# Performance work log

Hardware: AMD Instinct MI355X
Metric: run time of the kernel (lower is better)

## Reference

```python
import jax, jax.numpy as jnp
import numpy as np

N = 50000       # num nodes
E = 400000      # num edges (before self loops)
IN, HID, H, OUT = 128, 64, 4, 64
SLOPE = 0.2     # PyG GATv2Conv default negative_slope


def setup_inputs() -> dict:
    key = jax.random.key(0)
    ks = jax.random.split(key, 14)
    def lin(k, fan_in, fan_out):
        return jax.random.normal(k, (fan_in, fan_out), jnp.float32) / np.sqrt(fan_in)
    return {
        "x": jax.random.normal(ks[0], (N, IN), jnp.float32),
        "edge_index": jax.random.randint(ks[1], (2, E), 0, N, jnp.int32),
        # layer 1: in=IN -> HID per head, H heads, concat
        "Wl1": lin(ks[2], IN, H * HID), "bl1": jnp.zeros((H * HID,), jnp.float32),
        "Wr1": lin(ks[3], IN, H * HID), "br1": jnp.zeros((H * HID,), jnp.float32),
        "att1": jax.random.normal(ks[4], (H, HID), jnp.float32) / np.sqrt(HID),
        "bias1": jnp.zeros((H * HID,), jnp.float32),
        # layer 2: in=H*HID -> OUT, 1 head, concat=False
        "Wl2": lin(ks[5], H * HID, OUT), "bl2": jnp.zeros((OUT,), jnp.float32),
        "Wr2": lin(ks[6], H * HID, OUT), "br2": jnp.zeros((OUT,), jnp.float32),
        "att2": jax.random.normal(ks[7], (1, OUT), jnp.float32) / np.sqrt(OUT),
        "bias2": jnp.zeros((OUT,), jnp.float32),
    }


def gatv2_conv(x, src, dst, Wl, bl, Wr, br, att, heads, out_ch, num_nodes):
    """PyG GATv2Conv (share_weights=False). src->dst aggregation at dst."""
    xl = (x @ Wl + bl).reshape(-1, heads, out_ch)  # source transform (x_j)
    xr = (x @ Wr + br).reshape(-1, heads, out_ch)  # target transform (x_i)
    m = xl[src] + xr[dst]                          # [E, H, C]
    e = jnp.sum(jax.nn.leaky_relu(m, SLOPE) * att, axis=-1)  # [E, H]
    # segment softmax over incoming edges of each dst node
    emax = jax.ops.segment_max(e, dst, num_segments=num_nodes)
    ex = jnp.exp(e - emax[dst])
    denom = jax.ops.segment_sum(ex, dst, num_segments=num_nodes)
    alpha = ex / denom[dst]                        # [E, H]
    out = jax.ops.segment_sum(alpha[:, :, None] * xl[src], dst, num_segments=num_nodes)
    return out  # [N, H, C]


def reference(x, edge_index, Wl1, bl1, Wr1, br1, att1, bias1,
              Wl2, bl2, Wr2, br2, att2, bias2):
    n = x.shape[0]
    loops = jnp.arange(n, dtype=edge_index.dtype)
    src = jnp.concatenate([edge_index[0], loops])  # add_self_loops=True
    dst = jnp.concatenate([edge_index[1], loops])
    h = gatv2_conv(x, src, dst, Wl1, bl1, Wr1, br1, att1, H, HID, n)
    h = h.reshape(n, H * HID) + bias1              # concat=True
    h = jax.nn.elu(h)                              # dropout=0.0
    o = gatv2_conv(h, src, dst, Wl2, bl2, Wr2, br2, att2, 1, OUT, n)
    return o.reshape(n, OUT) + bias2               # concat=False, heads=1
```

## Files before the change

kernel.cpp:

```cpp
#include <hip/hip_runtime.h>
#include <hip/hip_bf16.h>

typedef unsigned short u16;
typedef __attribute__((ext_vector_type(8))) short short8;
typedef __attribute__((ext_vector_type(4))) float floatx4;
typedef __attribute__((ext_vector_type(2))) float f32x2;

#define N_NODES 50000
#define N_EDGES 400000
#define ET      450000
#define F_IN    128
#define C1      256
#define HID     64
#define OUTC    64
#define SLOPE   0.2f
#define LIN1_BLOCKS 391
#define LOG2E   1.44269504089f

#if __has_builtin(__builtin_amdgcn_exp2f)
#define EXP2(x) __builtin_amdgcn_exp2f(x)
#else
#define EXP2(x) __expf((x) * 0.69314718056f)
#endif

__device__ __forceinline__ float bf2f(u16 v) {
    return __uint_as_float(((unsigned)v) << 16);
}
__device__ __forceinline__ float bflo(unsigned u) { return __uint_as_float(u << 16); }
__device__ __forceinline__ float bfhi(unsigned u) { return __uint_as_float(u & 0xffff0000u); }
__device__ __forceinline__ u16 f2bf(float f) {
    unsigned u = __float_as_uint(f);
    return (u16)((u + 0x7fffu + ((u >> 16) & 1u)) >> 16);
}
__device__ __forceinline__ f32x2 up2(unsigned u) {
    f32x2 r; r.x = bflo(u); r.y = bfhi(u); return r;
}
template<int CTRL>
__device__ __forceinline__ float dpp_add(float x) {
    return x + __int_as_float(__builtin_amdgcn_update_dpp(
        0, __float_as_int(x), CTRL, 0xF, 0xF, true));
}
__device__ __forceinline__ float red16(float p) {
    p = dpp_add<0xB1>(p);
    p = dpp_add<0x4E>(p);
    p = dpp_add<0x141>(p);
    p = dpp_add<0x140>(p);
    return p;
}
template<int CTRL>
__device__ __forceinline__ f32x2 dpp_add2(f32x2 x) {
    f32x2 o;
    o.x = __int_as_float(__builtin_amdgcn_update_dpp(
        0, __float_as_int(x.x), CTRL, 0xF, 0xF, true));
    o.y = __int_as_float(__builtin_amdgcn_update_dpp(
        0, __float_as_int(x.y), CTRL, 0xF, 0xF, true));
    return x + o;
}
__device__ __forceinline__ f32x2 red16x2(f32x2 p) {
    p = dpp_add2<0xB1>(p);
    p = dpp_add2<0x4E>(p);
    p = dpp_add2<0x141>(p);
    p = dpp_add2<0x140>(p);
    return p;
}
__device__ __forceinline__ bool detect_f32(const unsigned* __restrict__ xw) {
    unsigned w = xw[threadIdx.x & 63];
    unsigned aexp = (w >> 7) & 0xFFu;
    unsigned long long b = __ballot(aexp >= 170u || aexp <= 40u);
    return __popcll(b) >= 16;
}

__global__ __launch_bounds__(256) void convert_all_kernel(
    const unsigned* __restrict__ xw,
    const void* wl1, const void* wr1, const void* wl2, const void* wr2,
    const void* s0, const void* s1, const void* s2, const void* s3,
    const void* s4, const void* s5, const void* s6, const void* s7,
    u16* __restrict__ wt, u16* __restrict__ prm, int* __restrict__ hist)
{
    if (blockIdx.x >= 385) {
        int idx = (blockIdx.x - 385) * 256 + threadIdx.x;
        if (idx < N_NODES) hist[idx] = 0;
        return;
    }
    bool f32m = detect_f32(xw);
    if (blockIdx.x == 384) {
        for (int t = threadIdx.x; t < 1280; t += 256) {
            const void* src; int local;
            if      (t < 256)  { src = s0; local = t; }
            else if (t < 512)  { src = s1; local = t - 256; }
            else if (t < 768)  { src = s2; local = t - 512; }
            else if (t < 1024) { src = s3; local = t - 768; }
            else if (t < 1088) { src = s4; local = t - 1024; }
            else if (t < 1152) { src = s5; local = t - 1088; }
            else if (t < 1216) { src = s6; local = t - 1152; }
            else               { src = s7; local = t - 1216; }
            prm[t] = f32m ? f2bf(((const float*)src)[local]) : ((const u16*)src)[local];
        }
        return;
    }
    int t = blockIdx.x * 256 + threadIdx.x;
    const void* src; int local, k, n, K, base;
    if (t < 32768)      { src = wl1; local = t;         k = local >> 8; n = local & 255; K = 128; base = 0; }
    else if (t < 65536) { src = wr1; local = t - 32768; k = local >> 8; n = local & 255; K = 128; base = 32768; }
    else if (t < 81920) { src = wl2; local = t - 65536; k = local >> 6; n = local & 63;  K = 256; base = 65536; }
    else                { src = wr2; local = t - 81920; k = local >> 6; n = local & 63;  K = 256; base = 81920; }
    u16 v = f32m ? f2bf(((const float*)src)[local]) : ((const u16*)src)[local];
    wt[base + n * K + k] = v;
}

__global__ __launch_bounds__(256) void scan1_kernel(const int* __restrict__ hist,
                                                    int* __restrict__ rowptr,
                                                    int* __restrict__ bsum)
{
    int t = threadIdx.x;
    int i = blockIdx.x * 256 + t;
    int v = (i < N_NODES) ? hist[i] : 0;
    __shared__ int sd[256];
    sd[t] = v;
    __syncthreads();
    #pragma unroll
    for (int ofs = 1; ofs < 256; ofs <<= 1) {
        int u = (t >= ofs) ? sd[t - ofs] : 0;
        __syncthreads();
        sd[t] += u;
        __syncthreads();
    }
    if (i < N_NODES) rowptr[i] = sd[t] - v;
    if (t == 255) bsum[blockIdx.x] = sd[255];
}

__global__ __launch_bounds__(256) void scan3_kernel(int* __restrict__ rowptr,
                                                    const int* __restrict__ bsum,
                                                    int* __restrict__ off)
{
    int t = threadIdx.x;
    int v = (t < (int)blockIdx.x) ? bsum[t] : 0;
    __shared__ int sd[256];
    sd[t] = v;
    __syncthreads();
    #pragma unroll
    for (int ofs = 1; ofs < 256; ofs <<= 1) {
        int u = (t >= ofs) ? sd[t - ofs] : 0;
        __syncthreads();
        sd[t] += u;
        __syncthreads();
    }
    int boff = sd[255];
    int i = blockIdx.x * 256 + t;
    if (i < N_NODES) {
        int r = rowptr[i] + boff;
        rowptr[i] = r;
        off[i] = r;
    }
}

__global__ __launch_bounds__(256) void scatter_kernel(const int* __restrict__ ei,
                                                      int* __restrict__ off,
                                                      int* __restrict__ src_csr)
{
    int t = blockIdx.x * 256 + threadIdx.x;
    if (t >= ET) return;
    int s, d;
    if (t < N_EDGES) { s = ei[t]; d = ei[N_EDGES + t]; } else { s = d = t - N_EDGES; }
    int pos = atomicAdd(&off[d], 1);
    src_csr[pos] = s;
}

__global__ __launch_bounds__(256) void lin1_hist_kernel(
    const u16* __restrict__ X, const u16* __restrict__ Wt,
    const u16* __restrict__ bl, const u16* __restrict__ br,
    u16* __restrict__ Yl, u16* __restrict__ Yr, int nrows,
    const int* __restrict__ ei, int* __restrict__ hist)
{
    constexpr int K = 128, N = 256, LS = K + 8, RB = 128;
    __shared__ __align__(16) u16 sX[RB * LS];
    __shared__ __align__(16) u16 sW[64 * LS];

    if (blockIdx.x >= LIN1_BLOCKS) {
        int t = (blockIdx.x - LIN1_BLOCKS) * 256 + threadIdx.x;
        if (t < ET) {
            int d = (t < N_EDGES) ? ei[N_EDGES + t] : t - N_EDGES;
            atomicAdd(&hist[d], 1);
        }
        return;
    }

    const bool f32m = detect_f32((const unsigned*)X);
    const float* X32 = (const float*)X;
    const int row0 = blockIdx.x * RB;
    const int wave = threadIdx.x >> 6, lane = threadIdx.x & 63;
    const int quad = lane >> 4, l16 = lane & 15;

    for (int i = threadIdx.x * 8; i < RB * K; i += 2048) {
        int r = i >> 7, c = i & 127;
        int gr = row0 + r;
        u16* dst = &sX[r * LS + c];
        if (f32m) {
            float4 v0 = make_float4(0.f, 0.f, 0.f, 0.f), v1 = v0;
            if (gr < nrows) {
                v0 = *(const float4*)&X32[(size_t)gr * K + c];
                v1 = *(const float4*)&X32[(size_t)gr * K + c + 4];
            }
            ushort4 p0, p1;
            p0.x = f2bf(v0.x); p0.y = f2bf(v0.y); p0.z = f2bf(v0.z); p0.w = f2bf(v0.w);
            p1.x = f2bf(v1.x); p1.y = f2bf(v1.y); p1.z = f2bf(v1.z); p1.w = f2bf(v1.w);
            *(ushort4*)dst = p0;
            *(ushort4*)(dst + 4) = p1;
        } else {
            uint4 v = {0u, 0u, 0u, 0u};
            if (gr < nrows) v = *(const uint4*)&X[(size_t)gr * K + c];
            *(uint4*)dst = v;
        }
    }
    __syncthreads();

    short8 a[2][4];
    #pragma unroll
    for (int t = 0; t < 2; ++t)
        #pragma unroll
        for (int kk = 0; kk < 4; ++kk)
            a[t][kk] = *(const short8*)&sX[(wave * 32 + t * 16 + l16) * LS + kk * 32 + quad * 8];

    for (int side = 0; side < 2; ++side) {
        const u16* wbase = Wt + side * (N * K);
        const u16* bias  = side ? br : bl;
        u16* Y = side ? Yr : Yl;
        for (int ch = 0; ch < 4; ++ch) {
            __syncthreads();
            for (int i = threadIdx.x * 8; i < 64 * K; i += 2048) {
                int n = i >> 7, c = i & 127;
                *(uint4*)&sW[n * LS + c] = *(const uint4*)&wbase[(size_t)(ch * 64 + n) * K + c];
            }
            __syncthreads();
            floatx4 acc[2][4];
            #pragma unroll
            for (int t = 0; t < 2; ++t)
                #pragma unroll
                for (int cf = 0; cf < 4; ++cf)
                    acc[t][cf] = (floatx4){0.f, 0.f, 0.f, 0.f};
            #pragma unroll
            for (int kk = 0; kk < 4; ++kk) {
                short8 b0 = *(const short8*)&sW[(l16) * LS + kk * 32 + quad * 8];
                short8 b1 = *(const short8*)&sW[(16 + l16) * LS + kk * 32 + quad * 8];
                short8 b2 = *(const short8*)&sW[(32 + l16) * LS + kk * 32 + quad * 8];
                short8 b3 = *(const short8*)&sW[(48 + l16) * LS + kk * 32 + quad * 8];
                #pragma unroll
                for (int t = 0; t < 2; ++t) {
                    acc[t][0] = __builtin_amdgcn_mfma_f32_16x16x32_bf16(a[t][kk], b0, acc[t][0], 0, 0, 0);
                    acc[t][1] = __builtin_amdgcn_mfma_f32_16x16x32_bf16(a[t][kk], b1, acc[t][1], 0, 0, 0);
                    acc[t][2] = __builtin_amdgcn_mfma_f32_16x16x32_bf16(a[t][kk], b2, acc[t][2], 0, 0, 0);
                    acc[t][3] = __builtin_amdgcn_mfma_f32_16x16x32_bf16(a[t][kk], b3, acc[t][3], 0, 0, 0);
                }
            }
            #pragma unroll
            for (int t = 0; t < 2; ++t) {
                const int rbase = row0 + wave * 32 + t * 16 + quad * 4;
                #pragma unroll
                for (int cf = 0; cf < 4; ++cf) {
                    const floatx4 av = acc[t][cf];
                    const int col = ch * 64 + cf * 16 + l16;
                    const float bv = bf2f(bias[col]);
                    #pragma unroll
                    for (int r = 0; r < 4; ++r) {
                        int row = rbase + r;
                        if (row < nrows) Y[(size_t)row * N + col] = f2bf(av[r] + bv);
                    }
                }
            }
        }
    }
}

__global__ __launch_bounds__(256) void lin2_fused_kernel(
    const u16* __restrict__ X, const u16* __restrict__ Wt,
    const u16* __restrict__ bl, const u16* __restrict__ br,
    u16* __restrict__ Yl, u16* __restrict__ Yr, int nrows)
{
    constexpr int K = 256, N = 64, LS = K + 8;
    __shared__ __align__(16) u16 sX[64 * LS];
    __shared__ __align__(16) u16 sW[64 * LS];
    const int row0 = blockIdx.x * 64;
    const int wave = threadIdx.x >> 6, lane = threadIdx.x & 63;
    const int quad = lane >> 4, l16 = lane & 15;

    for (int i = threadIdx.x * 8; i < 64 * K; i += 2048) {
        int r = i >> 8, c = i & 255;
        int gr = row0 + r;
        uint4 v = {0u, 0u, 0u, 0u};
        if (gr < nrows) v = *(const uint4*)&X[(size_t)gr * K + c];
        *(uint4*)&sX[r * LS + c] = v;
    }
    __syncthreads();

    short8 a[8];
    #pragma unroll
    for (int kk = 0; kk < 8; ++kk)
        a[kk] = *(const short8*)&sX[(wave * 16 + l16) * LS + kk * 32 + quad * 8];

    for (int side = 0; side < 2; ++side) {
        const u16* wbase = Wt + side * (N * K);
        const u16* bias  = side ? br : bl;
        u16* Y = side ? Yr : Yl;
        __syncthreads();
        for (int i = threadIdx.x * 8; i < 64 * K; i += 2048) {
            int n = i >> 8, c = i & 255;
            *(uint4*)&sW[n * LS + c] = *(const uint4*)&wbase[(size_t)n * K + c];
        }
        __syncthreads();
        floatx4 acc0 = {0.f, 0.f, 0.f, 0.f}, acc1 = acc0, acc2 = acc0, acc3 = acc0;
        #pragma unroll
        for (int kk = 0; kk < 8; ++kk) {
            short8 b0 = *(const short8*)&sW[(l16) * LS + kk * 32 + quad * 8];
            short8 b1 = *(const short8*)&sW[(16 + l16) * LS + kk * 32 + quad * 8];
            short8 b2 = *(const short8*)&sW[(32 + l16) * LS + kk * 32 + quad * 8];
            short8 b3 = *(const short8*)&sW[(48 + l16) * LS + kk * 32 + quad * 8];
            acc0 = __builtin_amdgcn_mfma_f32_16x16x32_bf16(a[kk], b0, acc0, 0, 0, 0);
            acc1 = __builtin_amdgcn_mfma_f32_16x16x32_bf16(a[kk], b1, acc1, 0, 0, 0);
            acc2 = __builtin_amdgcn_mfma_f32_16x16x32_bf16(a[kk], b2, acc2, 0, 0, 0);
            acc3 = __builtin_amdgcn_mfma_f32_16x16x32_bf16(a[kk], b3, acc3, 0, 0, 0);
        }
        const int rbase = row0 + wave * 16 + quad * 4;
        #pragma unroll
        for (int cf = 0; cf < 4; ++cf) {
            const floatx4 av = (cf == 0) ? acc0 : (cf == 1) ? acc1 : (cf == 2) ? acc2 : acc3;
            const int col = cf * 16 + l16;
            const float bv = bf2f(bias[col]);
            #pragma unroll
            for (int r = 0; r < 4; ++r) {
                int row = rbase + r;
                if (row < nrows) Y[(size_t)row * N + col] = f2bf(av[r] + bv);
            }
        }
    }
}

__global__ __launch_bounds__(64, 6) void node1_kernel(
    const u16* __restrict__ xl, const u16* __restrict__ xr,
    const int* __restrict__ rowptr, const int* __restrict__ hist,
    const int* __restrict__ src_csr, const u16* __restrict__ att,
    const u16* __restrict__ bias, u16* __restrict__ hout)
{
    const int d = blockIdx.x;
    const int l = threadIdx.x;
    const int start = rowptr[d];
    const int deg = hist[d];
    const int dm1 = deg - 1;
    const u16* __restrict__ xlp = xl + l * 4;

    uint2 auv = *(const uint2*)&att[l * 4];
    const f32x2 atA = up2(auv.x) * LOG2E, atB = up2(auv.y) * LOG2E;
    uint2 ruv = *(const uint2*)&xr[(size_t)d * C1 + l * 4];
    const f32x2 rA = up2(ruv.x), rB = up2(ruv.y);

    float m = -1e30f, la = 0.f;
    f32x2 accA = {0.f, 0.f}, accB = {0.f, 0.f};

    int s0 = src_csr[start];
    int s1 = src_csr[start + min(1, dm1)];
    int s2 = src_csr[start + min(2, dm1)];
    int s3 = src_csr[start + min(3, dm1)];
    uint2 u0 = *(const uint2*)&xlp[(size_t)s0 * C1];
    uint2 u1 = *(const uint2*)&xlp[(size_t)s1 * C1];
    uint2 u2 = *(const uint2*)&xlp[(size_t)s2 * C1];
    uint2 u3 = *(const uint2*)&xlp[(size_t)s3 * C1];

    int j = 0;
    for (; j + 4 <= deg; j += 4) {
        const uint2 c0 = u0, c1 = u1, c2 = u2, c3 = u3;
        const int jn = j + 4;
        if (jn < deg) {
            int t0 = src_csr[start + jn];
            int t1 = src_csr[start + min(jn + 1, dm1)];
            int t2 = src_csr[start + min(jn + 2, dm1)];
            int t3 = src_csr[start + min(jn + 3, dm1)];
            u0 = *(const uint2*)&xlp[(size_t)t0 * C1];
            u1 = *(const uint2*)&xlp[(size_t)t1 * C1];
            u2 = *(const uint2*)&xlp[(size_t)t2 * C1];
            u3 = *(const uint2*)&xlp[(size_t)t3 * C1];
        }
        f32x2 x0A = up2(c0.x), x0B = up2(c0.y);
        f32x2 x1A = up2(c1.x), x1B = up2(c1.y);
        f32x2 x2A = up2(c2.x), x2B = up2(c2.y);
        f32x2 x3A = up2(c3.x), x3B = up2(c3.y);
        f32x2 t, pv;
        t = x0A + rA; t = __builtin_elementwise_max(t, t * SLOPE); pv  = t * atA;
        t = x0B + rB; t = __builtin_elementwise_max(t, t * SLOPE); pv += t * atB;
        float p0 = pv.x + pv.y;
        t = x1A + rA; t = __builtin_elementwise_max(t, t * SLOPE); pv  = t * atA;
        t = x1B + rB; t = __builtin_elementwise_max(t, t * SLOPE); pv += t * atB;
        float p1 = pv.x + pv.y;
        t = x2A + rA; t = __builtin_elementwise_max(t, t * SLOPE); pv  = t * atA;
        t = x2B + rB; t = __builtin_elementwise_max(t, t * SLOPE); pv += t * atB;
        float p2 = pv.x + pv.y;
        t = x3A + rA; t = __builtin_elementwise_max(t, t * SLOPE); pv  = t * atA;
        t = x3B + rB; t = __builtin_elementwise_max(t, t * SLOPE); pv += t * atB;
        float p3 = pv.x + pv.y;
        f32x2 P01 = {p0, p1}, P23 = {p2, p3};
        P01 = red16x2(P01);
        P23 = red16x2(P23);
        p0 = P01.x; p1 = P01.y; p2 = P23.x; p3 = P23.y;
        float pm = fmaxf(fmaxf(p0, p1), fmaxf(p2, p3));
        if (__any(pm > m)) {
            float mn = fmaxf(m, pm);
            float sc = EXP2(m - mn);
            la *= sc; accA *= sc; accB *= sc;
            m = mn;
        }
        float w0 = EXP2(p0 - m);
        float w1 = EXP2(p1 - m);
        float w2 = EXP2(p2 - m);
        float w3 = EXP2(p3 - m);
        la += w0 + w1 + w2 + w3;
        accA += x0A * w0 + x1A * w1 + x2A * w2 + x3A * w3;
        accB += x0B * w0 + x1B * w1 + x2B * w2 + x3B * w3;
    }
    if (j < deg) {
        const bool v1 = j + 1 < deg, v2 = j + 2 < deg;
        f32x2 x0A = up2(u0.x), x0B = up2(u0.y);
        f32x2 x1A = up2(u1.x), x1B = up2(u1.y);
        f32x2 x2A = up2(u2.x), x2B = up2(u2.y);
        f32x2 t, pv;
        t = x0A + rA; t = __builtin_elementwise_max(t, t * SLOPE); pv  = t * atA;
        t = x0B + rB; t = __builtin_elementwise_max(t, t * SLOPE); pv += t * atB;
        float p0 = pv.x + pv.y;
        t = x1A + rA; t = __builtin_elementwise_max(t, t * SLOPE); pv  = t * atA;
        t = x1B + rB; t = __builtin_elementwise_max(t, t * SLOPE); pv += t * atB;
        float p1 = pv.x + pv.y;
        t = x2A + rA; t = __builtin_elementwise_max(t, t * SLOPE); pv  = t * atA;
        t = x2B + rB; t = __builtin_elementwise_max(t, t * SLOPE); pv += t * atB;
        float p2 = pv.x + pv.y;
        f32x2 P01 = {p0, p1};
        P01 = red16x2(P01);
        p0 = P01.x; p1 = P01.y;
        p2 = red16(p2);
        float pm = p0;
        if (v1) pm = fmaxf(pm, p1);
        if (v2) pm = fmaxf(pm, p2);
        if (__any(pm > m)) {
            float mn = fmaxf(m, pm);
            float sc = EXP2(m - mn);
            la *= sc; accA *= sc; accB *= sc;
            m = mn;
        }
        float w0 = EXP2(p0 - m);
        float w1 = v1 ? EXP2(p1 - m) : 0.f;
        float w2 = v2 ? EXP2(p2 - m) : 0.f;
        la += w0 + w1 + w2;
        accA += x0A * w0 + x1A * w1 + x2A * w2;
        accB += x0B * w0 + x1B * w1 + x2B * w2;
    }
    const float inv = 1.f / la;
    const int c = l * 4;
    float v0 = accA.x * inv + bf2f(bias[c + 0]);
    float v1 = accA.y * inv + bf2f(bias[c + 1]);
    float v2 = accB.x * inv + bf2f(bias[c + 2]);
    float v3 = accB.y * inv + bf2f(bias[c + 3]);
    v0 = v0 > 0.f ? v0 : __expf(fminf(v0, 0.f)) - 1.f;
    v1 = v1 > 0.f ? v1 : __expf(fminf(v1, 0.f)) - 1.f;
    v2 = v2 > 0.f ? v2 : __expf(fminf(v2, 0.f)) - 1.f;
    v3 = v3 > 0.f ? v3 : __expf(fminf(v3, 0.f)) - 1.f;
    ushort4 o;
    o.x = f2bf(v0); o.y = f2bf(v1); o.z = f2bf(v2); o.w = f2bf(v3);
    *(ushort4*)&hout[(size_t)d * C1 + c] = o;
}

__global__ __launch_bounds__(64, 8) void node2_kernel(
    const u16* __restrict__ xl, const u16* __restrict__ xr,
    const int* __restrict__ rowptr, const int* __restrict__ hist,
    const int* __restrict__ src_csr, const u16* __restrict__ att,
    const u16* __restrict__ bias, void* __restrict__ outp,
    const unsigned* __restrict__ xorig)
{
    const bool f32o = detect_f32(xorig);
    const int d = blockIdx.x;
    const int l = threadIdx.x;
    const int start = rowptr[d];
    const int deg = hist[d];
    const int dm1 = deg - 1;
    const int g = l >> 4, sub = l & 15;
    const int c0 = sub * 4;
    const u16* __restrict__ xlp = xl + c0;

    uint2 auv = *(const uint2*)&att[c0];
    const f32x2 atA = up2(auv.x) * LOG2E, atB = up2(auv.y) * LOG2E;
    uint2 ruv = *(const uint2*)&xr[(size_t)d * OUTC + c0];
    const f32x2 rA = up2(ruv.x), rB = up2(ruv.y);

    float m = -1e30f, la = 0.f;
    f32x2 accA = {0.f, 0.f}, accB = {0.f, 0.f};

    int sA = src_csr[start + min(g, dm1)];
    uint2 uA = *(const uint2*)&xlp[(size_t)sA * OUTC];
    int sB = src_csr[start + min(4 + g, dm1)];
    uint2 uB = *(const uint2*)&xlp[(size_t)sB * OUTC];

    for (int j = 0; j < deg; j += 4) {
        const bool valid = j + g < deg;
        const uint2 uv = uA;
        uA = uB;
        {
            int sC = src_csr[start + min(j + 8 + g, dm1)];
            uB = *(const uint2*)&xlp[(size_t)sC * OUTC];
        }
        f32x2 xA = up2(uv.x), xB = up2(uv.y);
        f32x2 t, pv;
        t = xA + rA; t = __builtin_elementwise_max(t, t * SLOPE); pv  = t * atA;
        t = xB + rB; t = __builtin_elementwise_max(t, t * SLOPE); pv += t * atB;
        float p = pv.x + pv.y;
        p = red16(p);
        float pvv = valid ? p : -1e30f;
        if (__any(pvv > m)) {
            float mn = fmaxf(m, pvv);
            float sc = EXP2(m - mn);
            la *= sc; accA *= sc; accB *= sc;
            m = mn;
        }
        float w = valid ? EXP2(p - m) : 0.f;
        la += w;
        accA += xA * w;
        accB += xB * w;
    }
    #pragma unroll
    for (int ofs = 16; ofs <= 32; ofs <<= 1) {
        float mo = __shfl_xor(m, ofs);
        float lo = __shfl_xor(la, ofs);
        float bax = __shfl_xor(accA.x, ofs);
        float bay = __shfl_xor(accA.y, ofs);
        float bbx = __shfl_xor(accB.x, ofs);
        float bby = __shfl_xor(accB.y, ofs);
        float mn = fmaxf(m, mo);
        float e0 = EXP2(m - mn), e1 = EXP2(mo - mn);
        la = la * e0 + lo * e1;
        accA.x = accA.x * e0 + bax * e1;
        accA.y = accA.y * e0 + bay * e1;
        accB.x = accB.x * e0 + bbx * e1;
        accB.y = accB.y * e0 + bby * e1;
        m = mn;
    }
    if (g == 0) {
        const float inv = 1.f / la;
        float v0 = accA.x * inv + bf2f(bias[c0 + 0]);
        float v1 = accA.y * inv + bf2f(bias[c0 + 1]);
        float v2 = accB.x * inv + bf2f(bias[c0 + 2]);
        float v3 = accB.y * inv + bf2f(bias[c0 + 3]);
        if (f32o) {
            float4 o = make_float4(v0, v1, v2, v3);
            *(float4*)&((float*)outp)[(size_t)d * OUTC + c0] = o;
        } else {
            ushort4 o;
            o.x = f2bf(v0); o.y = f2bf(v1); o.z = f2bf(v2); o.w = f2bf(v3);
            *(ushort4*)&((u16*)outp)[(size_t)d * OUTC + c0] = o;
        }
    }
}

extern "C" void kernel_launch(void* const* d_in, const int* in_sizes, int n_in,
                              void* d_out, int out_size, void* d_ws, size_t ws_size,
                              hipStream_t stream)
{
    const void* x  = d_in[0];
    const int*  ei = (const int*)d_in[1];

    char* ws = (char*)d_ws;
    u16* xl1     = (u16*)(ws + 0);
    u16* xr1     = (u16*)(ws + 25600000);
    u16* hbuf    = (u16*)(ws + 51200000);
    u16* xl2     = (u16*)(ws + 0);
    u16* xr2     = (u16*)(ws + 6400000);
    int* hist    = (int*)(ws + 76800000);
    int* rowptr  = (int*)(ws + 77000000);
    int* off     = (int*)(ws + 77200000);
    int* src_csr = (int*)(ws + 77400000);
    u16* prm     = (u16*)(ws + 79200064);
    u16* wt      = (u16*)(ws + 79210240);
    int* bsum    = (int*)(ws + 79410000);

    u16* bl1   = prm + 0;
    u16* br1   = prm + 256;
    u16* att1  = prm + 512;
    u16* bias1 = prm + 768;
    u16* bl2   = prm + 1024;
    u16* br2   = prm + 1088;
    u16* att2  = prm + 1152;
    u16* bias2 = prm + 1216;
    u16* wt1   = wt + 0;
    u16* wt2   = wt + 65536;

    convert_all_kernel<<<581, 256, 0, stream>>>(
        (const unsigned*)x,
        d_in[2], d_in[4], d_in[8], d_in[10],
        d_in[3], d_in[5], d_in[6], d_in[7], d_in[9], d_in[11], d_in[12], d_in[13],
        wt, prm, hist);

    const int eb = (ET + 255) / 256;
    lin1_hist_kernel<<<LIN1_BLOCKS + eb, 256, 0, stream>>>(
        (const u16*)x, wt1, bl1, br1, xl1, xr1, N_NODES, ei, hist);

    scan1_kernel<<<196, 256, 0, stream>>>(hist, rowptr, bsum);
    scan3_kernel<<<196, 256, 0, stream>>>(rowptr, bsum, off);
    scatter_kernel<<<eb, 256, 0, stream>>>(ei, off, src_csr);

    node1_kernel<<<N_NODES, 64, 0, stream>>>(xl1, xr1, rowptr, hist, src_csr, att1, bias1, hbuf);
    lin2_fused_kernel<<<(N_NODES + 63) / 64, 256, 0, stream>>>(hbuf, wt2, bl2, br2, xl2, xr2, N_NODES);
    node2_kernel<<<N_NODES, 64, 0, stream>>>(xl2, xr2, rowptr, hist, src_csr, att2, bias2, d_out,
                                             (const unsigned*)x);
}
```

Baseline: 249.4 us.

## Split lin1 GEMM blocks by side and row tile; use scalar CSR indices

The layer-1 projection kernel now launches one block per 64-row tile per side (left or right weights) instead of one block per 128-row tile computing both sides. This raises the block count fourfold so the 256 CUs are better filled, at the cost of each input tile being loaded twice. The node kernels also wrap the rowptr, degree and CSR source-index loads in readfirstlane, so the compiler can treat them as wave-uniform scalars and reduce vector register and address work. LIN1_BLOCKS is redefined to 782 but is no longer used.

```diff
diff --git a/kernel.cpp b/kernel.cpp
--- a/kernel.cpp
+++ b/kernel.cpp
@@ -14,7 +14,8 @@
 #define HID     64
 #define OUTC    64
 #define SLOPE   0.2f
-#define LIN1_BLOCKS 391
+#define LIN1_BLOCKS 782
+#define LIN1_GEMM   1564
 #define LOG2E   1.44269504089f
 
 #if __has_builtin(__builtin_amdgcn_exp2f)
@@ -172,12 +173,12 @@
     u16* __restrict__ Yl, u16* __restrict__ Yr, int nrows,
     const int* __restrict__ ei, int* __restrict__ hist)
 {
-    constexpr int K = 128, N = 256, LS = K + 8, RB = 128;
-    __shared__ __align__(16) u16 sX[RB * LS];
+    constexpr int K = 128, N = 256, LS = K + 8;
+    __shared__ __align__(16) u16 sX[64 * LS];
     __shared__ __align__(16) u16 sW[64 * LS];
 
-    if (blockIdx.x >= LIN1_BLOCKS) {
-        int t = (blockIdx.x - LIN1_BLOCKS) * 256 + threadIdx.x;
+    if (blockIdx.x >= LIN1_GEMM) {
+        int t = (blockIdx.x - LIN1_GEMM) * 256 + threadIdx.x;
         if (t < ET) {
             int d = (t < N_EDGES) ? ei[N_EDGES + t] : t - N_EDGES;
             atomicAdd(&hist[d], 1);
@@ -187,11 +188,12 @@
 
     const bool f32m = detect_f32((const unsigned*)X);
     const float* X32 = (const float*)X;
-    const int row0 = blockIdx.x * RB;
+    const int side = blockIdx.x & 1;
+    const int row0 = (blockIdx.x >> 1) * 64;
     const int wave = threadIdx.x >> 6, lane = threadIdx.x & 63;
     const int quad = lane >> 4, l16 = lane & 15;
 
-    for (int i = threadIdx.x * 8; i < RB * K; i += 2048) {
+    for (int i = threadIdx.x * 8; i < 64 * K; i += 2048) {
         int r = i >> 7, c = i & 127;
         int gr = row0 + r;
         u16* dst = &sX[r * LS + c];
@@ -214,58 +216,43 @@
     }
     __syncthreads();
 
-    short8 a[2][4];
+    short8 a[4];
     #pragma unroll
-    for (int t = 0; t < 2; ++t)
+    for (int kk = 0; kk < 4; ++kk)
+        a[kk] = *(const short8*)&sX[(wave * 16 + l16) * LS + kk * 32 + quad * 8];
+
+    const u16* wbase = Wt + side * (N * K);
+    const u16* bias  = side ? br : bl;
+    u16* Y = side ? Yr : Yl;
+    for (int ch = 0; ch < 4; ++ch) {
+        if (ch) __syncthreads();
+        for (int i = threadIdx.x * 8; i < 64 * K; i += 2048) {
+            int n = i >> 7, c = i & 127;
+            *(uint4*)&sW[n * LS + c] = *(const uint4*)&wbase[(size_t)(ch * 64 + n) * K + c];
+        }
+        __syncthreads();
+        floatx4 acc0 = {0.f, 0.f, 0.f, 0.f}, acc1 = acc0, acc2 = acc0, acc3 = acc0;
         #pragma unroll
-        for (int kk = 0; kk < 4; ++kk)
-            a[t][kk] = *(const short8*)&sX[(wave * 32 + t * 16 + l16) * LS + kk * 32 + quad * 8];
-
-    for (int side = 0; side < 2; ++side) {
-        const u16* wbase = Wt + side * (N * K);
-        const u16* bias  = side ? br : bl;
-        u16* Y = side ? Yr : Yl;
-        for (int ch = 0; ch < 4; ++ch) {
-            __syncthreads();
-            for (int i = threadIdx.x * 8; i < 64 * K; i += 2048) {
-                int n = i >> 7, c = i & 127;
-                *(uint4*)&sW[n * LS + c] = *(const uint4*)&wbase[(size_t)(ch * 64 + n) * K + c];
-            }
-            __syncthreads();
-            floatx4 acc[2][4];
+        for (int kk = 0; kk < 4; ++kk) {
+            short8 b0 = *(const short8*)&sW[(l16) * LS + kk * 32 + quad * 8];
+            short8 b1 = *(const short8*)&sW[(16 + l16) * LS + kk * 32 + quad * 8];
+            short8 b2 = *(const short8*)&sW[(32 + l16) * LS + kk * 32 + quad * 8];
+            short8 b3 = *(const short8*)&sW[(48 + l16) * LS + kk * 32 + quad * 8];
+            acc0 = __builtin_amdgcn_mfma_f32_16x16x32_bf16(a[kk], b0, acc0, 0, 0, 0);
+            acc1 = __builtin_amdgcn_mfma_f32_16x16x32_bf16(a[kk], b1, acc1, 0, 0, 0);
+            acc2 = __builtin_amdgcn_mfma_f32_16x16x32_bf16(a[kk], b2, acc2, 0, 0, 0);
+            acc3 = __builtin_amdgcn_mfma_f32_16x16x32_bf16(a[kk], b3, acc3, 0, 0, 0);
+        }
+        const int rbase = row0 + wave * 16 + quad * 4;
+        #pragma unroll
+        for (int cf = 0; cf < 4; ++cf) {
+            const floatx4 av = (cf == 0) ? acc0 : (cf == 1) ? acc1 : (cf == 2) ? acc2 : acc3;
+            const int col = ch * 64 + cf * 16 + l16;
+            const float bv = bf2f(bias[col]);
             #pragma unroll
-            for (int t = 0; t < 2; ++t)
-                #pragma unroll
-                for (int cf = 0; cf < 4; ++cf)
-                    acc[t][cf] = (floatx4){0.f, 0.f, 0.f, 0.f};
-            #pragma unroll
-            for (int kk = 0; kk < 4; ++kk) {
-                short8 b0 = *(const short8*)&sW[(l16) * LS + kk * 32 + quad * 8];
-                short8 b1 = *(const short8*)&sW[(16 + l16) * LS + kk * 32 + quad * 8];
-                short8 b2 = *(const short8*)&sW[(32 + l16) * LS + kk * 32 + quad * 8];
-                short8 b3 = *(const short8*)&sW[(48 + l16) * LS + kk * 32 + quad * 8];
-                #pragma unroll
-                for (int t = 0; t < 2; ++t) {
-                    acc[t][0] = __builtin_amdgcn_mfma_f32_16x16x32_bf16(a[t][kk], b0, acc[t][0], 0, 0, 0);
-                    acc[t][1] = __builtin_amdgcn_mfma_f32_16x16x32_bf16(a[t][kk], b1, acc[t][1], 0, 0, 0);
-                    acc[t][2] = __builtin_amdgcn_mfma_f32_16x16x32_bf16(a[t][kk], b2, acc[t][2], 0, 0, 0);
-                    acc[t][3] = __builtin_amdgcn_mfma_f32_16x16x32_bf16(a[t][kk], b3, acc[t][3], 0, 0, 0);
-                }
-            }
-            #pragma unroll
-            for (int t = 0; t < 2; ++t) {
-                const int rbase = row0 + wave * 32 + t * 16 + quad * 4;
-                #pragma unroll
-                for (int cf = 0; cf < 4; ++cf) {
-                    const floatx4 av = acc[t][cf];
-                    const int col = ch * 64 + cf * 16 + l16;
-                    const float bv = bf2f(bias[col]);
-                    #pragma unroll
-                    for (int r = 0; r < 4; ++r) {
-                        int row = rbase + r;
-                        if (row < nrows) Y[(size_t)row * N + col] = f2bf(av[r] + bv);
-                    }
-                }
+            for (int r = 0; r < 4; ++r) {
+                int row = rbase + r;
+                if (row < nrows) Y[(size_t)row * N + col] = f2bf(av[r] + bv);
             }
         }
     }
@@ -342,8 +329,8 @@
 {
     const int d = blockIdx.x;
     const int l = threadIdx.x;
-    const int start = rowptr[d];
-    const int deg = hist[d];
+    const int start = __builtin_amdgcn_readfirstlane(rowptr[d]);
+    const int deg = __builtin_amdgcn_readfirstlane(hist[d]);
     const int dm1 = deg - 1;
     const u16* __restrict__ xlp = xl + l * 4;
 
@@ -355,10 +342,10 @@
     float m = -1e30f, la = 0.f;
     f32x2 accA = {0.f, 0.f}, accB = {0.f, 0.f};
 
-    int s0 = src_csr[start];
-    int s1 = src_csr[start + min(1, dm1)];
-    int s2 = src_csr[start + min(2, dm1)];
-    int s3 = src_csr[start + min(3, dm1)];
+    int s0 = __builtin_amdgcn_readfirstlane(src_csr[start]);
+    int s1 = __builtin_amdgcn_readfirstlane(src_csr[start + min(1, dm1)]);
+    int s2 = __builtin_amdgcn_readfirstlane(src_csr[start + min(2, dm1)]);
+    int s3 = __builtin_amdgcn_readfirstlane(src_csr[start + min(3, dm1)]);
     uint2 u0 = *(const uint2*)&xlp[(size_t)s0 * C1];
     uint2 u1 = *(const uint2*)&xlp[(size_t)s1 * C1];
     uint2 u2 = *(const uint2*)&xlp[(size_t)s2 * C1];
@@ -369,10 +356,10 @@
         const uint2 c0 = u0, c1 = u1, c2 = u2, c3 = u3;
         const int jn = j + 4;
         if (jn < deg) {
-            int t0 = src_csr[start + jn];
-            int t1 = src_csr[start + min(jn + 1, dm1)];
-            int t2 = src_csr[start + min(jn + 2, dm1)];
-            int t3 = src_csr[start + min(jn + 3, dm1)];
+            int t0 = __builtin_amdgcn_readfirstlane(src_csr[start + jn]);
+            int t1 = __builtin_amdgcn_readfirstlane(src_csr[start + min(jn + 1, dm1)]);
+            int t2 = __builtin_amdgcn_readfirstlane(src_csr[start + min(jn + 2, dm1)]);
+            int t3 = __builtin_amdgcn_readfirstlane(src_csr[start + min(jn + 3, dm1)]);
             u0 = *(const uint2*)&xlp[(size_t)t0 * C1];
             u1 = *(const uint2*)&xlp[(size_t)t1 * C1];
             u2 = *(const uint2*)&xlp[(size_t)t2 * C1];
@@ -474,8 +461,8 @@
     const bool f32o = detect_f32(xorig);
     const int d = blockIdx.x;
     const int l = threadIdx.x;
-    const int start = rowptr[d];
-    const int deg = hist[d];
+    const int start = __builtin_amdgcn_readfirstlane(rowptr[d]);
+    const int deg = __builtin_amdgcn_readfirstlane(hist[d]);
     const int dm1 = deg - 1;
     const int g = l >> 4, sub = l & 15;
     const int c0 = sub * 4;
@@ -593,7 +580,7 @@
         wt, prm, hist);
 
     const int eb = (ET + 255) / 256;
-    lin1_hist_kernel<<<LIN1_BLOCKS + eb, 256, 0, stream>>>(
+    lin1_hist_kernel<<<LIN1_GEMM + eb, 256, 0, stream>>>(
         (const u16*)x, wt1, bl1, br1, xl1, xr1, N_NODES, ei, hist);
 
     scan1_kernel<<<196, 256, 0, stream>>>(hist, rowptr, bsum);
```

Result: no change. 249.7 us (+0.1%).
